# Kernel tuning notes

Hardware: AMD Instinct MI355X
Metric: run time of the kernel (lower is better)

Reference implementation:

```python
import jax, jax.numpy as jnp
import numpy as np

SEQ, BATCH, IN_DIM, HID = 2048, 32, 512, 512


def setup_inputs() -> dict:
    key = jax.random.key(0)
    ks = jax.random.split(key, 5)
    scale_ih = 1.0 / np.sqrt(HID)
    return {
        "x": jax.random.normal(ks[0], (SEQ, BATCH, IN_DIM), dtype=jnp.float32),
        "h0": jnp.zeros((BATCH, HID), dtype=jnp.float32),
        "c0": jnp.zeros((BATCH, HID), dtype=jnp.float32),
        "W_ih": jax.random.uniform(ks[1], (4 * HID, IN_DIM), dtype=jnp.float32, minval=-scale_ih, maxval=scale_ih),
        "W_hh": jax.random.uniform(ks[2], (4 * HID, HID), dtype=jnp.float32, minval=-scale_ih, maxval=scale_ih),
        "b_ih": jax.random.uniform(ks[3], (4 * HID,), dtype=jnp.float32, minval=-scale_ih, maxval=scale_ih),
        "b_hh": jax.random.uniform(ks[4], (4 * HID,), dtype=jnp.float32, minval=-scale_ih, maxval=scale_ih),
    }


def reference(x, h0, c0, W_ih, W_hh, b_ih, b_hh):
    # torch.nn.LSTMCell gate order: input, forget, cell(g), output
    b = b_ih + b_hh
    # Precompute input projections for all timesteps: [S, B, 4H]
    x_proj = jnp.einsum("sbi,gi->sbg", x, W_ih) + b

    def step(carry, xp_t):
        h, c = carry
        gates = xp_t + h @ W_hh.T  # [B, 4H]
        i, f, g, o = jnp.split(gates, 4, axis=-1)
        i = jax.nn.sigmoid(i)
        f = jax.nn.sigmoid(f)
        g = jnp.tanh(g)
        o = jax.nn.sigmoid(o)
        c_new = f * c + i * g
        h_new = o * jnp.tanh(c_new)
        return (h_new, c_new), h_new

    (h_T, c_T), hs = jax.lax.scan(step, (h0, c0), x_proj)
    return hs, h_T, c_T
```

## Files before the change

kernel.cpp:

```cpp
#include <hip/hip_runtime.h>
#include <math.h>

#define SEQ    2048
#define BATCH  32
#define IN_DIM 512
#define HID    512
#define GATES  (4*HID)

typedef __attribute__((ext_vector_type(4))) float f32x4;

__global__ __launch_bounds__(256) void xproj_kernel(
    const float* __restrict__ x,
    const float* __restrict__ Wih,
    const float* __restrict__ bih,
    const float* __restrict__ bhh,
    float* __restrict__ xp,
    int M)
{
    __shared__ float As[16][132];
    __shared__ float Bs[16][132];
    const int tid = threadIdx.x;
    const int nb = blockIdx.x & 15;
    const int mb = blockIdx.x >> 4;
    const int m0 = mb * 128, n0 = nb * 128;
    const int tx = tid & 15, ty = tid >> 4;

    float acc[8][8];
#pragma unroll
    for (int i = 0; i < 8; ++i)
#pragma unroll
        for (int j = 0; j < 8; ++j) acc[i][j] = 0.f;

    for (int kc = 0; kc < 512; kc += 16) {
#pragma unroll
        for (int h = 0; h < 2; ++h) {
            int f4 = tid + 256 * h;
            int r = f4 >> 2, u = f4 & 3;
            float4 va = *(const float4*)(x + (size_t)(m0 + r) * 512 + kc + 4 * u);
            As[4*u+0][r] = va.x; As[4*u+1][r] = va.y;
            As[4*u+2][r] = va.z; As[4*u+3][r] = va.w;
            float4 vb = *(const float4*)(Wih + (size_t)(n0 + r) * 512 + kc + 4 * u);
            Bs[4*u+0][r] = vb.x; Bs[4*u+1][r] = vb.y;
            Bs[4*u+2][r] = vb.z; Bs[4*u+3][r] = vb.w;
        }
        __syncthreads();
#pragma unroll
        for (int kk = 0; kk < 16; ++kk) {
            float4 a0 = *(const float4*)&As[kk][tx * 8];
            float4 a1 = *(const float4*)&As[kk][tx * 8 + 4];
            float4 b0 = *(const float4*)&Bs[kk][ty * 8];
            float4 b1 = *(const float4*)&Bs[kk][ty * 8 + 4];
            float av[8] = {a0.x,a0.y,a0.z,a0.w,a1.x,a1.y,a1.z,a1.w};
            float bv[8] = {b0.x,b0.y,b0.z,b0.w,b1.x,b1.y,b1.z,b1.w};
#pragma unroll
            for (int i = 0; i < 8; ++i)
#pragma unroll
                for (int j = 0; j < 8; ++j) acc[i][j] += av[i] * bv[j];
        }
        __syncthreads();
    }

    float bias[8];
#pragma unroll
    for (int j = 0; j < 8; ++j) {
        int n = n0 + ty * 8 + j;
        bias[j] = bih[n] + bhh[n];
    }
#pragma unroll
    for (int i = 0; i < 8; ++i) {
        size_t base = (size_t)(m0 + tx * 8 + i) * GATES + n0 + ty * 8;
        float4 v0 = make_float4(acc[i][0]+bias[0], acc[i][1]+bias[1],
                                acc[i][2]+bias[2], acc[i][3]+bias[3]);
        float4 v1 = make_float4(acc[i][4]+bias[4], acc[i][5]+bias[5],
                                acc[i][6]+bias[6], acc[i][7]+bias[7]);
        *(float4*)(xp + base)     = v0;
        *(float4*)(xp + base + 4) = v1;
    }
}

__global__ __launch_bounds__(256, 1) void lstm_coop(
    const float* __restrict__ Whh,
    const float* __restrict__ xp,
    float* __restrict__ hbuf,
    float* __restrict__ cbuf,
    unsigned* __restrict__ flags,
    float* __restrict__ out_hs,
    int t0, int nsteps)
{
    const int w    = blockIdx.x;
    const int g    = w >> 5;
    const int sl   = w & 31;
    const int tid  = threadIdx.x;
    const int gate = tid >> 6;
    const int lane = tid & 63;
    const int hid_h = lane >> 4;
    const int kg    = lane & 15;
    const int hid0  = 16 * sl;
    const int B0    = 4 * g;

    __shared__ f32x4 h4[512];
    __shared__ float gbuf[4][64];

    float wreg[4][32];
#pragma unroll
    for (int i = 0; i < 4; ++i) {
        const float* wr = Whh + (size_t)(512 * gate + hid0 + 4 * hid_h + i) * 512
                          + 32 * kg;
#pragma unroll
        for (int q = 0; q < 8; ++q) {
            float4 v = *(const float4*)(wr + 4 * q);
            wreg[i][4*q+0] = v.x; wreg[i][4*q+1] = v.y;
            wreg[i][4*q+2] = v.z; wreg[i][4*q+3] = v.w;
        }
    }

    float c_reg = 0.f;
    if (tid < 64) {
        int hid_local = 4 * (tid >> 4) + ((tid >> 2) & 3);
        int b_j = tid & 3;
        c_reg = cbuf[(size_t)(B0 + b_j) * HID + hid0 + hid_local];
    }

    unsigned* const gflags = flags + g * 1024;

    for (int t = t0; t < t0 + nsteps; ++t) {
        const int xrow = 512 * gate + hid0 + 4 * hid_h + (kg >> 2);
        const int xb   = B0 + (kg & 3);
        float xpv = xp[(size_t)(t - t0) * (BATCH * GATES)
                       + (size_t)xb * GATES + xrow];

        {
            const unsigned* fp = gflags + (lane & 31) * 32;
            const unsigned target = (unsigned)t;
            while (true) {
                unsigned v;
                asm volatile("global_load_dword %0, %1, off sc0 sc1\n\t"
                             "s_waitcnt vmcnt(0)"
                             : "=&v"(v) : "v"(fp) : "memory");
                bool stale = (lane < 32) && (v < target);
                if (__ballot(stale) == 0ull) break;
                __builtin_amdgcn_s_sleep(1);
            }
        }

        {
            const float* hsrc = hbuf + ((size_t)(t & 1) * 8 + g) * 2048;
            f32x4 v0, v1;
            asm volatile("global_load_dwordx4 %0, %2, off sc0 sc1\n\t"
                         "global_load_dwordx4 %1, %3, off sc0 sc1\n\t"
                         "s_waitcnt vmcnt(0)"
                         : "=&v"(v0), "=&v"(v1)
                         : "v"(hsrc + 4 * tid), "v"(hsrc + 4 * (tid + 256))
                         : "memory");
            h4[tid]       = v0;
            h4[tid + 256] = v1;
        }
        __syncthreads();

        float acc[16];
#pragma unroll
        for (int m = 0; m < 16; ++m) acc[m] = 0.f;
#pragma unroll
        for (int s = 0; s < 32; ++s) {
            f32x4 hv = h4[16 * s + kg];
#pragma unroll
            for (int i = 0; i < 4; ++i) {
                acc[4*i+0] += wreg[i][s] * hv[0];
                acc[4*i+1] += wreg[i][s] * hv[1];
                acc[4*i+2] += wreg[i][s] * hv[2];
                acc[4*i+3] += wreg[i][s] * hv[3];
            }
        }

        {
            int sel = (kg >> 3) & 1;
#pragma unroll
            for (int m = 0; m < 8; ++m) {
                float mine = sel ? acc[m+8] : acc[m];
                float send = sel ? acc[m]   : acc[m+8];
                acc[m] = mine + __shfl_xor(send, 8, 64);
            }
        }
        {
            int sel = (kg >> 2) & 1;
#pragma unroll
            for (int m = 0; m < 4; ++m) {
                float mine = sel ? acc[m+4] : acc[m];
                float send = sel ? acc[m]   : acc[m+4];
                acc[m] = mine + __shfl_xor(send, 4, 64);
            }
        }
        {
            int sel = (kg >> 1) & 1;
#pragma unroll
            for (int m = 0; m < 2; ++m) {
                float mine = sel ? acc[m+2] : acc[m];
                float send = sel ? acc[m]   : acc[m+2];
                acc[m] = mine + __shfl_xor(send, 2, 64);
            }
        }
        {
            int sel = kg & 1;
            float mine = sel ? acc[1] : acc[0];
            float send = sel ? acc[0] : acc[1];
            acc[0] = mine + __shfl_xor(send, 1, 64);
        }

        gbuf[gate][lane] = acc[0] + xpv;
        __syncthreads();

        if (tid < 64) {
            float iv = gbuf[0][tid];
            float fv = gbuf[1][tid];
            float gv = gbuf[2][tid];
            float ov = gbuf[3][tid];
            iv = 1.f / (1.f + expf(-iv));
            fv = 1.f / (1.f + expf(-fv));
            ov = 1.f / (1.f + expf(-ov));
            gv = tanhf(gv);
            float cn = fv * c_reg + iv * gv;
            float hn = ov * tanhf(cn);
            c_reg = cn;

            int hid_local = 4 * (tid >> 4) + ((tid >> 2) & 3);
            int b_j = tid & 3;
            int k = hid0 + hid_local;
            int slot = 16 * (k & 31) + (k >> 5);
            float* hp = hbuf + ((size_t)((t + 1) & 1) * 8 + g) * 2048
                        + 4 * slot + b_j;
            asm volatile("global_store_dword %0, %1, off sc0 sc1"
                         :: "v"(hp), "v"(hn) : "memory");
            asm volatile("s_waitcnt vmcnt(0)" ::: "memory");
            if (tid == 0) {
                unsigned fv2 = (unsigned)(t + 1);
                unsigned* fp = gflags + sl * 32;
                asm volatile("global_store_dword %0, %1, off sc0 sc1"
                             :: "v"(fp), "v"(fv2) : "memory");
            }
            out_hs[(size_t)t * (BATCH * HID) + (size_t)(B0 + b_j) * HID + k] = hn;
        }
    }

    if (tid < 64) {
        int hid_local = 4 * (tid >> 4) + ((tid >> 2) & 3);
        int b_j = tid & 3;
        cbuf[(size_t)(B0 + b_j) * HID + hid0 + hid_local] = c_reg;
    }
}

__global__ void init_kernel(const float* __restrict__ h0,
                            const float* __restrict__ c0,
                            float* __restrict__ hbuf,
                            float* __restrict__ cbuf,
                            unsigned* __restrict__ flags)
{
    int idx = blockIdx.x * 256 + threadIdx.x;
    if (idx < BATCH * HID) {
        int b = idx >> 9, k = idx & 511;
        int g = b >> 2, b_j = b & 3;
        int slot = 16 * (k & 31) + (k >> 5);
        hbuf[(size_t)g * 2048 + 4 * slot + b_j] = h0[idx];
        cbuf[idx] = c0[idx];
    }
    if (idx < 8192) flags[idx] = 0u;
}

__global__ void tail_kernel(const float* __restrict__ hbuf,
                            const float* __restrict__ cbuf,
                            float* __restrict__ out)
{
    int idx = blockIdx.x * 256 + threadIdx.x;
    if (idx < BATCH * HID) {
        int b = idx >> 9, k = idx & 511;
        int g = b >> 2, b_j = b & 3;
        int slot = 16 * (k & 31) + (k >> 5);
        out[(size_t)SEQ * BATCH * HID + idx] =
            hbuf[(size_t)g * 2048 + 4 * slot + b_j];
        out[(size_t)SEQ * BATCH * HID + BATCH * HID + idx] = cbuf[idx];
    }
}

extern "C" void kernel_launch(void* const* d_in, const int* in_sizes, int n_in,
                              void* d_out, int out_size, void* d_ws, size_t ws_size,
                              hipStream_t stream)
{
    const float* x   = (const float*)d_in[0];
    const float* h0  = (const float*)d_in[1];
    const float* c0  = (const float*)d_in[2];
    const float* Wih = (const float*)d_in[3];
    const float* Whh = (const float*)d_in[4];
    const float* bih = (const float*)d_in[5];
    const float* bhh = (const float*)d_in[6];
    float* out = (float*)d_out;

    float*    hbuf  = (float*)d_ws;
    float*    cbuf  = hbuf + 32768;
    unsigned* flags = (unsigned*)(cbuf + 16384);
    float*    xp    = (float*)(flags + 8192);
    size_t used_floats = 32768 + 16384 + 8192;
    size_t avail = (ws_size / 4 > used_floats) ? (ws_size / 4 - used_floats) : 0;
    int chunk = (int)(avail / (size_t)(BATCH * GATES));
    if (chunk > SEQ) chunk = SEQ;
    chunk &= ~3;
    if (chunk < 4) chunk = 4;

    hipLaunchKernelGGL(init_kernel, dim3(64), dim3(256), 0, stream,
                       h0, c0, hbuf, cbuf, flags);

    for (int t0 = 0; t0 < SEQ; t0 += chunk) {
        int n = SEQ - t0; if (n > chunk) n = chunk;
        int M = n * BATCH;
        hipLaunchKernelGGL(xproj_kernel, dim3(16 * (M / 128)), dim3(256), 0, stream,
                           x + (size_t)t0 * BATCH * IN_DIM, Wih, bih, bhh, xp, M);

        const float* xp_c = xp;
        int t0_arg = t0, n_arg = n;
        void* args[] = { (void*)&Whh, (void*)&xp_c, (void*)&hbuf, (void*)&cbuf,
                         (void*)&flags, (void*)&out, (void*)&t0_arg, (void*)&n_arg };
        hipLaunchCooperativeKernel((void*)lstm_coop, dim3(256), dim3(256),
                                   args, 0, stream);
    }

    hipLaunchKernelGGL(tail_kernel, dim3(64), dim3(256), 0, stream,
                       hbuf, cbuf, out);
}
```

Baseline: 9.611 ms.

## Tag h values with step number to replace flag polling and remove LDS gate exchange

After: 10.30 ms. +7.1%, slower.

```diff
diff --git a/kernel.cpp b/kernel.cpp
--- a/kernel.cpp
+++ b/kernel.cpp
@@ -8,6 +8,7 @@
 #define GATES  (4*HID)
 
 typedef __attribute__((ext_vector_type(4))) float f32x4;
+typedef __attribute__((ext_vector_type(2))) float f32x2;
 
 __global__ __launch_bounds__(256) void xproj_kernel(
     const float* __restrict__ x,
@@ -78,12 +79,13 @@
     }
 }
 
-__global__ __launch_bounds__(256, 1) void lstm_coop(
+__global__ __launch_bounds__(256, 1)
+__attribute__((amdgpu_waves_per_eu(1, 1)))
+void lstm_coop(
     const float* __restrict__ Whh,
     const float* __restrict__ xp,
-    float* __restrict__ hbuf,
+    float* __restrict__ hx,
     float* __restrict__ cbuf,
-    unsigned* __restrict__ flags,
     float* __restrict__ out_hs,
     int t0, int nsteps)
 {
@@ -91,69 +93,73 @@
     const int g    = w >> 5;
     const int sl   = w & 31;
     const int tid  = threadIdx.x;
-    const int gate = tid >> 6;
+    const int hw   = tid >> 6;
     const int lane = tid & 63;
-    const int hid_h = lane >> 4;
-    const int kg    = lane & 15;
-    const int hid0  = 16 * sl;
-    const int B0    = 4 * g;
-
-    __shared__ f32x4 h4[512];
-    __shared__ float gbuf[4][64];
+    const int rr   = (lane >> 4) & 3;
+    const int kg   = lane & 15;
+
+    __shared__ f32x4 h4[2][512];
 
     float wreg[4][32];
 #pragma unroll
-    for (int i = 0; i < 4; ++i) {
-        const float* wr = Whh + (size_t)(512 * gate + hid0 + 4 * hid_h + i) * 512
-                          + 32 * kg;
+    for (int gi = 0; gi < 4; ++gi) {
+        const float* wr = Whh + (size_t)(512*gi + 16*sl + 4*hw + rr) * 512 + 32*kg;
 #pragma unroll
         for (int q = 0; q < 8; ++q) {
-            float4 v = *(const float4*)(wr + 4 * q);
-            wreg[i][4*q+0] = v.x; wreg[i][4*q+1] = v.y;
-            wreg[i][4*q+2] = v.z; wreg[i][4*q+3] = v.w;
-        }
-    }
+            float4 v = *(const float4*)(wr + 4*q);
+            wreg[gi][4*q+0] = v.x; wreg[gi][4*q+1] = v.y;
+            wreg[gi][4*q+2] = v.z; wreg[gi][4*q+3] = v.w;
+        }
+    }
+
+    const bool is_tail = ((lane & 12) == 0);
+    const int  jb      = lane & 3;
+    const int  hid_gl  = 16*sl + 4*hw + rr;
+    const int  b_gl    = 4*g + jb;
+    const int  slot_p  = 16*(hid_gl & 31) + (hid_gl >> 5);
 
     float c_reg = 0.f;
-    if (tid < 64) {
-        int hid_local = 4 * (tid >> 4) + ((tid >> 2) & 3);
-        int b_j = tid & 3;
-        c_reg = cbuf[(size_t)(B0 + b_j) * HID + hid0 + hid_local];
-    }
-
-    unsigned* const gflags = flags + g * 1024;
+    if (is_tail) c_reg = cbuf[(size_t)b_gl * HID + hid_gl];
 
     for (int t = t0; t < t0 + nsteps; ++t) {
-        const int xrow = 512 * gate + hid0 + 4 * hid_h + (kg >> 2);
-        const int xb   = B0 + (kg & 3);
+        const int p = t & 1;
+        const int xrow = 512*(kg >> 2) + 16*sl + 4*hw + rr;
+        const int xb   = 4*g + (kg & 3);
         float xpv = xp[(size_t)(t - t0) * (BATCH * GATES)
                        + (size_t)xb * GATES + xrow];
 
-        {
-            const unsigned* fp = gflags + (lane & 31) * 32;
-            const unsigned target = (unsigned)t;
-            while (true) {
-                unsigned v;
-                asm volatile("global_load_dword %0, %1, off sc0 sc1\n\t"
-                             "s_waitcnt vmcnt(0)"
-                             : "=&v"(v) : "v"(fp) : "memory");
-                bool stale = (lane < 32) && (v < target);
-                if (__ballot(stale) == 0ull) break;
-                __builtin_amdgcn_s_sleep(1);
-            }
-        }
-
-        {
-            const float* hsrc = hbuf + ((size_t)(t & 1) * 8 + g) * 2048;
-            f32x4 v0, v1;
-            asm volatile("global_load_dwordx4 %0, %2, off sc0 sc1\n\t"
-                         "global_load_dwordx4 %1, %3, off sc0 sc1\n\t"
-                         "s_waitcnt vmcnt(0)"
-                         : "=&v"(v0), "=&v"(v1)
-                         : "v"(hsrc + 4 * tid), "v"(hsrc + 4 * (tid + 256))
-                         : "memory");
-            h4[tid]       = v0;
-            h4[tid + 256] = v1;
+        const float* rb = hx + ((size_t)p * 8 + g) * 4096;
+        const float* p0 = rb + 8 * tid;
+        const float* p1 = rb + 8 * tid + 2048;
+        const unsigned tu = __float_as_uint((float)t);
+        f32x2 a0, a1, a2, a3, b0, b1, b2, b3;
+        while (true) {
+            asm volatile(
+                "global_load_dwordx2 %0, %8, off sc0 sc1\n\t"
+                "global_load_dwordx2 %1, %8, off offset:8 sc0 sc1\n\t"
+                "global_load_dwordx2 %2, %8, off offset:16 sc0 sc1\n\t"
+                "global_load_dwordx2 %3, %8, off offset:24 sc0 sc1\n\t"
+                "global_load_dwordx2 %4, %9, off sc0 sc1\n\t"
+                "global_load_dwordx2 %5, %9, off offset:8 sc0 sc1\n\t"
+                "global_load_dwordx2 %6, %9, off offset:16 sc0 sc1\n\t"
+                "global_load_dwordx2 %7, %9, off offset:24 sc0 sc1\n\t"
+                "s_waitcnt vmcnt(0)"
+                : "=&v"(a0), "=&v"(a1), "=&v"(a2), "=&v"(a3),
+                  "=&v"(b0), "=&v"(b1), "=&v"(b2), "=&v"(b3)
+                : "v"(p0), "v"(p1)
+                : "memory");
+            if (__float_as_uint(a0[1]) == tu && __float_as_uint(a1[1]) == tu &&
+                __float_as_uint(a2[1]) == tu && __float_as_uint(a3[1]) == tu &&
+                __float_as_uint(b0[1]) == tu && __float_as_uint(b1[1]) == tu &&
+                __float_as_uint(b2[1]) == tu && __float_as_uint(b3[1]) == tu)
+                break;
+            __builtin_amdgcn_s_sleep(1);
+        }
+        {
+            f32x4 v0 = {a0[0], a1[0], a2[0], a3[0]};
+            f32x4 v1 = {b0[0], b1[0], b2[0], b3[0]};
+            h4[p][tid]       = v0;
+            h4[p][tid + 256] = v1;
         }
         __syncthreads();
 
@@ -162,13 +168,13 @@
         for (int m = 0; m < 16; ++m) acc[m] = 0.f;
 #pragma unroll
         for (int s = 0; s < 32; ++s) {
-            f32x4 hv = h4[16 * s + kg];
-#pragma unroll
-            for (int i = 0; i < 4; ++i) {
-                acc[4*i+0] += wreg[i][s] * hv[0];
-                acc[4*i+1] += wreg[i][s] * hv[1];
-                acc[4*i+2] += wreg[i][s] * hv[2];
-                acc[4*i+3] += wreg[i][s] * hv[3];
+            f32x4 hv = h4[p][16*s + kg];
+#pragma unroll
+            for (int gi = 0; gi < 4; ++gi) {
+                acc[4*gi+0] += wreg[gi][s] * hv[0];
+                acc[4*gi+1] += wreg[gi][s] * hv[1];
+                acc[4*gi+2] += wreg[gi][s] * hv[2];
+                acc[4*gi+3] += wreg[gi][s] * hv[3];
             }
         }
 
@@ -206,76 +212,63 @@
             acc[0] = mine + __shfl_xor(send, 1, 64);
         }
 
-        gbuf[gate][lane] = acc[0] + xpv;
-        __syncthreads();
-
-        if (tid < 64) {
-            float iv = gbuf[0][tid];
-            float fv = gbuf[1][tid];
-            float gv = gbuf[2][tid];
-            float ov = gbuf[3][tid];
-            iv = 1.f / (1.f + expf(-iv));
-            fv = 1.f / (1.f + expf(-fv));
-            ov = 1.f / (1.f + expf(-ov));
-            gv = tanhf(gv);
+        float gval = acc[0] + xpv;
+        float fv2 = __shfl(gval, (lane & 48) + 4  + jb);
+        float gv2 = __shfl(gval, (lane & 48) + 8  + jb);
+        float ov2 = __shfl(gval, (lane & 48) + 12 + jb);
+
+        if (is_tail) {
+            float iv = 1.f / (1.f + expf(-gval));
+            float fv = 1.f / (1.f + expf(-fv2));
+            float gv = tanhf(gv2);
+            float ov = 1.f / (1.f + expf(-ov2));
             float cn = fv * c_reg + iv * gv;
             float hn = ov * tanhf(cn);
             c_reg = cn;
-
-            int hid_local = 4 * (tid >> 4) + ((tid >> 2) & 3);
-            int b_j = tid & 3;
-            int k = hid0 + hid_local;
-            int slot = 16 * (k & 31) + (k >> 5);
-            float* hp = hbuf + ((size_t)((t + 1) & 1) * 8 + g) * 2048
-                        + 4 * slot + b_j;
-            asm volatile("global_store_dword %0, %1, off sc0 sc1"
-                         :: "v"(hp), "v"(hn) : "memory");
-            asm volatile("s_waitcnt vmcnt(0)" ::: "memory");
-            if (tid == 0) {
-                unsigned fv2 = (unsigned)(t + 1);
-                unsigned* fp = gflags + sl * 32;
-                asm volatile("global_store_dword %0, %1, off sc0 sc1"
-                             :: "v"(fp), "v"(fv2) : "memory");
-            }
-            out_hs[(size_t)t * (BATCH * HID) + (size_t)(B0 + b_j) * HID + k] = hn;
-        }
-    }
-
-    if (tid < 64) {
-        int hid_local = 4 * (tid >> 4) + ((tid >> 2) & 3);
-        int b_j = tid & 3;
-        cbuf[(size_t)(B0 + b_j) * HID + hid0 + hid_local] = c_reg;
-    }
+            f32x2 pkt;
+            pkt[0] = hn;
+            pkt[1] = (float)(t + 1);
+            float* wp = hx + ((size_t)((t + 1) & 1) * 8 + g) * 4096
+                        + 8 * slot_p + 2 * jb;
+            asm volatile("global_store_dwordx2 %0, %1, off sc0 sc1"
+                         :: "v"(wp), "v"(pkt) : "memory");
+            out_hs[(size_t)t * (BATCH * HID) + (size_t)b_gl * HID + hid_gl] = hn;
+        }
+    }
+
+    if (is_tail) cbuf[(size_t)b_gl * HID + hid_gl] = c_reg;
 }
 
 __global__ void init_kernel(const float* __restrict__ h0,
                             const float* __restrict__ c0,
-                            float* __restrict__ hbuf,
-                            float* __restrict__ cbuf,
-                            unsigned* __restrict__ flags)
+                            float* __restrict__ hx,
+                            float* __restrict__ cbuf)
+{
+    int idx = blockIdx.x * 256 + threadIdx.x;
+    if (idx < 16384) {
+        int g = idx >> 11, G = idx & 2047;
+        int slot = G >> 2, c = G & 3;
+        int k = 32 * (slot & 15) + (slot >> 4);
+        int b = 4 * g + c;
+        hx[(size_t)g * 4096 + 2*G]     = h0[(size_t)b * HID + k];
+        hx[(size_t)g * 4096 + 2*G + 1] = 0.0f;
+        hx[(size_t)32768 + (size_t)g * 4096 + 2*G]     = 0.0f;
+        hx[(size_t)32768 + (size_t)g * 4096 + 2*G + 1] = __uint_as_float(0xFFFFFFFFu);
+        cbuf[idx] = c0[idx];
+    }
+}
+
+__global__ void tail_kernel(const float* __restrict__ hx,
+                            const float* __restrict__ cbuf,
+                            float* __restrict__ out)
 {
     int idx = blockIdx.x * 256 + threadIdx.x;
     if (idx < BATCH * HID) {
         int b = idx >> 9, k = idx & 511;
-        int g = b >> 2, b_j = b & 3;
+        int g = b >> 2, c = b & 3;
         int slot = 16 * (k & 31) + (k >> 5);
-        hbuf[(size_t)g * 2048 + 4 * slot + b_j] = h0[idx];
-        cbuf[idx] = c0[idx];
-    }
-    if (idx < 8192) flags[idx] = 0u;
-}
-
-__global__ void tail_kernel(const float* __restrict__ hbuf,
-                            const float* __restrict__ cbuf,
-                            float* __restrict__ out)
-{
-    int idx = blockIdx.x * 256 + threadIdx.x;
-    if (idx < BATCH * HID) {
-        int b = idx >> 9, k = idx & 511;
-        int g = b >> 2, b_j = b & 3;
-        int slot = 16 * (k & 31) + (k >> 5);
-        out[(size_t)SEQ * BATCH * HID + idx] =
-            hbuf[(size_t)g * 2048 + 4 * slot + b_j];
+        int G = 4 * slot + c;
+        out[(size_t)SEQ * BATCH * HID + idx] = hx[(size_t)g * 4096 + 2*G];
         out[(size_t)SEQ * BATCH * HID + BATCH * HID + idx] = cbuf[idx];
     }
 }
@@ -293,11 +286,10 @@
     const float* bhh = (const float*)d_in[6];
     float* out = (float*)d_out;
 
-    float*    hbuf  = (float*)d_ws;
-    float*    cbuf  = hbuf + 32768;
-    unsigned* flags = (unsigned*)(cbuf + 16384);
-    float*    xp    = (float*)(flags + 8192);
-    size_t used_floats = 32768 + 16384 + 8192;
+    float* hx   = (float*)d_ws;
+    float* cbuf = hx + 65536;
+    float* xp   = cbuf + 16384;
+    size_t used_floats = 65536 + 16384;
     size_t avail = (ws_size / 4 > used_floats) ? (ws_size / 4 - used_floats) : 0;
     int chunk = (int)(avail / (size_t)(BATCH * GATES));
     if (chunk > SEQ) chunk = SEQ;
@@ -305,7 +297,7 @@
     if (chunk < 4) chunk = 4;
 
     hipLaunchKernelGGL(init_kernel, dim3(64), dim3(256), 0, stream,
-                       h0, c0, hbuf, cbuf, flags);
+                       h0, c0, hx, cbuf);
 
     for (int t0 = 0; t0 < SEQ; t0 += chunk) {
         int n = SEQ - t0; if (n > chunk) n = chunk;
@@ -315,12 +307,12 @@
 
         const float* xp_c = xp;
         int t0_arg = t0, n_arg = n;
-        void* args[] = { (void*)&Whh, (void*)&xp_c, (void*)&hbuf, (void*)&cbuf,
-                         (void*)&flags, (void*)&out, (void*)&t0_arg, (void*)&n_arg };
+        void* args[] = { (void*)&Whh, (void*)&xp_c, (void*)&hx, (void*)&cbuf,
+                         (void*)&out, (void*)&t0_arg, (void*)&n_arg };
         hipLaunchCooperativeKernel((void*)lstm_coop, dim3(256), dim3(256),
                                    args, 0, stream);
     }
 
     hipLaunchKernelGGL(tail_kernel, dim3(64), dim3(256), 0, stream,
-                       hbuf, cbuf, out);
-}
+                       hx, cbuf, out);
+}
```
